# Kernel optimization log

Measured on AMD Instinct MI355X. Metric: run time of the kernel, lower is better.

## Reference

```python
import jax, jax.numpy as jnp
import numpy as np

NEG_SLOPE = 0.2  # PyG GATConv default negative_slope


def _gat_layer(x, src, dst, W_src, W_dst, att_src, att_dst, bias, num_nodes):
    """Single-head GATConv (concat=True, heads=1, add_self_loops=False)."""
    h_src = x @ W_src                      # [N, C]
    h_dst = x @ W_dst                      # [N, C]
    a_src = h_src @ att_src                # [N]
    a_dst = h_dst @ att_dst                # [N]
    # per-edge attention logits: message j -> i uses a_src[j] + a_dst[i]
    e = jax.nn.leaky_relu(a_src[src] + a_dst[dst], NEG_SLOPE)  # [E]
    # numerically stable softmax over incoming edges of each destination
    m = jax.ops.segment_max(e, dst, num_segments=num_nodes)    # [N]
    ee = jnp.exp(e - m[dst])                                   # [E]
    denom = jax.ops.segment_sum(ee, dst, num_segments=num_nodes)  # [N]
    alpha = ee / denom[dst]                                    # [E]
    # attention-weighted scatter-add of source messages
    out = jax.ops.segment_sum(h_src[src] * alpha[:, None], dst,
                              num_segments=num_nodes)          # [N, C]
    return out + bias


def setup_inputs() -> dict:
    key = jax.random.key(0)
    ks = jax.random.split(key, 12)
    N, E, F_IN, HID, OUT = 100000, 1600000, 128, 128, 64
    inp = {
        "x": jax.random.normal(ks[0], (N, F_IN), dtype=jnp.float32),
        "edge_index": jax.random.randint(ks[1], (2, E), 0, N, dtype=jnp.int64
                                         if jax.config.jax_enable_x64 else jnp.int32),
        "W_src1": jax.random.normal(ks[2], (F_IN, HID), dtype=jnp.float32) / np.sqrt(F_IN),
        "W_dst1": jax.random.normal(ks[3], (F_IN, HID), dtype=jnp.float32) / np.sqrt(F_IN),
        "att_src1": jax.random.normal(ks[4], (HID,), dtype=jnp.float32) / np.sqrt(HID),
        "att_dst1": jax.random.normal(ks[5], (HID,), dtype=jnp.float32) / np.sqrt(HID),
        "b1": jnp.zeros((HID,), dtype=jnp.float32),
        "W_src2": jax.random.normal(ks[6], (HID, OUT), dtype=jnp.float32) / np.sqrt(HID),
        "W_dst2": jax.random.normal(ks[7], (HID, OUT), dtype=jnp.float32) / np.sqrt(HID),
        "att_src2": jax.random.normal(ks[8], (OUT,), dtype=jnp.float32) / np.sqrt(OUT),
        "att_dst2": jax.random.normal(ks[9], (OUT,), dtype=jnp.float32) / np.sqrt(OUT),
        "b2": jnp.zeros((OUT,), dtype=jnp.float32),
    }
    return inp


def reference(x, edge_index, W_src1, W_dst1, att_src1, att_dst1, b1,
              W_src2, W_dst2, att_src2, att_dst2, b2):
    N = x.shape[0]
    src, dst = edge_index[0], edge_index[1]
    h = _gat_layer(x, src, dst, W_src1, W_dst1, att_src1, att_dst1, b1, N)
    h = jax.nn.relu(h)
    out = _gat_layer(h, src, dst, W_src2, W_dst2, att_src2, att_dst2, b2, N)
    return out
```

## Files before the change

kernel.cpp:

```cpp
#include <hip/hip_runtime.h>

#define F_IN 128
#define NEG_SLOPE 0.2f
#define SCAN_CHUNK 2048
#define CH 4096

typedef __attribute__((ext_vector_type(8))) short bf16x8;
typedef __attribute__((ext_vector_type(4))) float f32x4;

__device__ inline unsigned short f2bf(float f) {
    unsigned int u = __float_as_uint(f);
    unsigned int r = (u + 0x7fffu + ((u >> 16) & 1u)) >> 16;
    return (unsigned short)r;
}
__device__ inline float bf2f(unsigned short h) { return __uint_as_float((unsigned int)h << 16); }
__device__ inline float bflo(unsigned int u) { return __uint_as_float(u << 16); }
__device__ inline float bfhi(unsigned int u) { return __uint_as_float(u & 0xffff0000u); }

__device__ inline int bswiz(int n, int k) {
    int ct = n >> 4, rlo = n & 15, kk = k >> 5, q = (k >> 3) & 3, j = k & 7;
    return (((ct * 4 + kk) * 64 + q * 16 + rlo) << 3) + j;
}

__global__ void k_prep(const float* __restrict__ Ws1, const float* __restrict__ Wd1,
                       const float* __restrict__ as1, const float* __restrict__ ad1,
                       const float* __restrict__ Ws2, const float* __restrict__ Wd2,
                       const float* __restrict__ as2, const float* __restrict__ ad2,
                       float* __restrict__ vecs,
                       unsigned short* __restrict__ w1hi, unsigned short* __restrict__ w1lo,
                       unsigned short* __restrict__ w2hi, unsigned short* __restrict__ w2lo) {
    int bid = blockIdx.x, tid = threadIdx.x;
    if (bid == 0 && tid < 128) {
        int f = tid;
        float s1 = 0.f, d1 = 0.f, s2 = 0.f, d2 = 0.f;
        for (int c = 0; c < 128; ++c) {
            s1 += Ws1[f * 128 + c] * as1[c];
            d1 += Wd1[f * 128 + c] * ad1[c];
        }
        for (int c = 0; c < 64; ++c) {
            s2 += Ws2[f * 64 + c] * as2[c];
            d2 += Wd2[f * 64 + c] * ad2[c];
        }
        vecs[f] = s1; vecs[128 + f] = d1; vecs[256 + f] = s2; vecs[384 + f] = d2;
    } else if (bid >= 1 && bid < 65) {
        int idx = (bid - 1) * 256 + tid;
        int n = idx >> 7, k = idx & 127;
        float w = Ws1[k * 128 + n];
        unsigned short h = f2bf(w);
        int si = bswiz(n, k);
        w1hi[si] = h;
        w1lo[si] = f2bf(w - bf2f(h));
    } else if (bid >= 65 && bid < 97) {
        int idx = (bid - 65) * 256 + tid;
        int n = idx >> 7, k = idx & 127;
        float w = Ws2[k * 64 + n];
        unsigned short h = f2bf(w);
        int si = bswiz(n, k);
        w2hi[si] = h;
        w2lo[si] = f2bf(w - bf2f(h));
    }
}


__global__ void k_bhist(const int* __restrict__ dsts, int* __restrict__ table,
                        int E, int NB, int nblk) {
    __shared__ int bins[512];
    int t = threadIdx.x, blk = blockIdx.x;
    for (int j = t; j < NB; j += 256) bins[j] = 0;
    __syncthreads();
    int base = blk * CH;
    #pragma unroll
    for (int k = 0; k < CH / 256; ++k) {
        int idx = base + k * 256 + t;
        if (idx < E) atomicAdd(&bins[dsts[idx] >> 8], 1);
    }
    __syncthreads();
    for (int j = t; j < NB; j += 256) table[(long long)j * nblk + blk] = bins[j];
}

__global__ void k_blocksum2(const int* __restrict__ in, int* __restrict__ bsum, int M) {
    __shared__ int sh[256];
    int t = threadIdx.x;
    long long base = (long long)blockIdx.x * SCAN_CHUNK + (long long)t * 8;
    int s = 0;
    #pragma unroll
    for (int k = 0; k < 8; ++k) {
        long long i = base + k;
        if (i < M) s += in[i];
    }
    sh[t] = s;
    __syncthreads();
    for (int off = 128; off; off >>= 1) {
        if (t < off) sh[t] += sh[t + off];
        __syncthreads();
    }
    if (t == 0) bsum[blockIdx.x] = sh[0];
}

__global__ void k_scan2(const int* __restrict__ in, const int* __restrict__ bsum,
                        int* __restrict__ out, int M) {
    __shared__ int sh[256];
    int t = threadIdx.x, bid = blockIdx.x;
    int pre = 0;
    for (int b = 0; b < bid; ++b) pre += bsum[b];
    long long base = (long long)bid * SCAN_CHUNK + (long long)t * 8;
    int loc[8];
    int s = 0;
    #pragma unroll
    for (int k = 0; k < 8; ++k) {
        long long i = base + k;
        int v = (i < M) ? in[i] : 0;
        loc[k] = s;
        s += v;
    }
    sh[t] = s;
    __syncthreads();
    for (int off = 1; off < 256; off <<= 1) {
        int tmp = (t >= off) ? sh[t - off] : 0;
        __syncthreads();
        sh[t] += tmp;
        __syncthreads();
    }
    int toff = pre + sh[t] - s;
    #pragma unroll
    for (int k = 0; k < 8; ++k) {
        long long i = base + k;
        if (i < M) out[i] = toff + loc[k];
    }
}

__global__ void k_bscat(const int* __restrict__ srcs, const int* __restrict__ dsts,
                        const int* __restrict__ tscan, int2* __restrict__ pairA,
                        int E, int NB, int nblk) {
    __shared__ int offs[512];
    int t = threadIdx.x, blk = blockIdx.x;
    for (int j = t; j < NB; j += 256) offs[j] = tscan[(long long)j * nblk + blk];
    __syncthreads();
    int base = blk * CH;
    #pragma unroll
    for (int k = 0; k < CH / 256; ++k) {
        int idx = base + k * 256 + t;
        if (idx < E) {
            int d = dsts[idx], s = srcs[idx];
            int p = atomicAdd(&offs[d >> 8], 1);
            int2 pr; pr.x = d; pr.y = s;
            pairA[p] = pr;
        }
    }
}

__global__ void k_bfin(const int2* __restrict__ pairA, const int* __restrict__ tscan,
                       int* __restrict__ perm, int* __restrict__ rowptr,
                       int NB, int nblk, int N, int E) {
    __shared__ int scnt[256];
    __shared__ int sh[256];
    __shared__ int sptr[256];
    int t = threadIdx.x, b = blockIdx.x;
    int beg = tscan[(long long)b * nblk];
    int end = (b + 1 < NB) ? tscan[(long long)(b + 1) * nblk] : E;
    scnt[t] = 0;
    __syncthreads();
    for (int i = beg + t; i < end; i += 256) {
        int2 p = pairA[i];
        atomicAdd(&scnt[p.x & 255], 1);
    }
    __syncthreads();
    int c = scnt[t];
    sh[t] = c;
    __syncthreads();
    for (int off = 1; off < 256; off <<= 1) {
        int tmp = (t >= off) ? sh[t - off] : 0;
        __syncthreads();
        sh[t] += tmp;
        __syncthreads();
    }
    int excl = sh[t] - c;
    int node = (b << 8) + t;
    if (node < N) rowptr[node] = beg + excl;
    sptr[t] = beg + excl;
    __syncthreads();
    for (int i = beg + t; i < end; i += 256) {
        int2 p = pairA[i];
        int pos = atomicAdd(&sptr[p.x & 255], 1);
        perm[pos] = p.y;
    }
    if (b == NB - 1 && t == 0) rowptr[N] = E;
}

template <int COLS, bool ABF16>
__launch_bounds__(256)
__global__ void k_gemm_mfma(const void* __restrict__ Xv,
                            const unsigned short* __restrict__ Bh,
                            const unsigned short* __restrict__ Bl,
                            const float* __restrict__ vecs_s,
                            const float* __restrict__ vecs_d,
                            unsigned short* __restrict__ H,
                            float* __restrict__ a_s, float* __restrict__ a_d, int N) {
    int tid = threadIdx.x;
    int wave = tid >> 6, lane = tid & 63;
    int q = lane >> 4, rlo = lane & 15;
    long long wrow0 = (long long)blockIdx.x * 128 + wave * 32;

    bf16x8 Ahi[2][4], Alo[2][4];
    #pragma unroll
    for (int rt = 0; rt < 2; ++rt) {
        long long r = wrow0 + rt * 16 + rlo;
        long long rr = (r < N) ? r : (long long)(N - 1);
        float ps = 0.f, pd = 0.f;
        #pragma unroll
        for (int kk = 0; kk < 4; ++kk) {
            int k0 = kk * 32 + q * 8;
            float xv[8];
            if constexpr (ABF16) {
                const unsigned short* Xu = (const unsigned short*)Xv;
                bf16x8 av = *(const bf16x8*)(Xu + rr * 128 + k0);
                Ahi[rt][kk] = av;
                #pragma unroll
                for (int j = 0; j < 8; ++j) xv[j] = bf2f((unsigned short)av[j]);
            } else {
                const float* Xf = (const float*)Xv;
                float4 x0 = *(const float4*)(Xf + rr * 128 + k0);
                float4 x1 = *(const float4*)(Xf + rr * 128 + k0 + 4);
                xv[0] = x0.x; xv[1] = x0.y; xv[2] = x0.z; xv[3] = x0.w;
                xv[4] = x1.x; xv[5] = x1.y; xv[6] = x1.z; xv[7] = x1.w;
                bf16x8 ah, al;
                #pragma unroll
                for (int j = 0; j < 8; ++j) {
                    unsigned short h = f2bf(xv[j]);
                    ah[j] = (short)h;
                    al[j] = (short)f2bf(xv[j] - bf2f(h));
                }
                Ahi[rt][kk] = ah; Alo[rt][kk] = al;
            }
            float4 vs0 = *(const float4*)(vecs_s + k0);
            float4 vs1 = *(const float4*)(vecs_s + k0 + 4);
            float4 vd0 = *(const float4*)(vecs_d + k0);
            float4 vd1 = *(const float4*)(vecs_d + k0 + 4);
            ps += xv[0] * vs0.x + xv[1] * vs0.y + xv[2] * vs0.z + xv[3] * vs0.w
                + xv[4] * vs1.x + xv[5] * vs1.y + xv[6] * vs1.z + xv[7] * vs1.w;
            pd += xv[0] * vd0.x + xv[1] * vd0.y + xv[2] * vd0.z + xv[3] * vd0.w
                + xv[4] * vd1.x + xv[5] * vd1.y + xv[6] * vd1.z + xv[7] * vd1.w;
        }
        ps += __shfl_xor(ps, 16); ps += __shfl_xor(ps, 32);
        pd += __shfl_xor(pd, 16); pd += __shfl_xor(pd, 32);
        if (q == 0 && r < N) { a_s[r] = ps; a_d[r] = pd; }
    }

    const bf16x8* Bh8 = (const bf16x8*)Bh;
    const bf16x8* Bl8 = (const bf16x8*)Bl;
    #pragma unroll 1
    for (int ct = 0; ct < COLS / 16; ++ct) {
        bf16x8 bh[4], bl[4];
        #pragma unroll
        for (int kk = 0; kk < 4; ++kk) {
            bh[kk] = Bh8[(ct * 4 + kk) * 64 + lane];
            bl[kk] = Bl8[(ct * 4 + kk) * 64 + lane];
        }
        f32x4 acc0 = {0.f, 0.f, 0.f, 0.f};
        f32x4 acc1 = {0.f, 0.f, 0.f, 0.f};
        #pragma unroll
        for (int kk = 0; kk < 4; ++kk) {
            acc0 = __builtin_amdgcn_mfma_f32_16x16x32_bf16(Ahi[0][kk], bh[kk], acc0, 0, 0, 0);
            acc1 = __builtin_amdgcn_mfma_f32_16x16x32_bf16(Ahi[1][kk], bh[kk], acc1, 0, 0, 0);
            if constexpr (!ABF16) {
                acc0 = __builtin_amdgcn_mfma_f32_16x16x32_bf16(Alo[0][kk], bh[kk], acc0, 0, 0, 0);
                acc1 = __builtin_amdgcn_mfma_f32_16x16x32_bf16(Alo[1][kk], bh[kk], acc1, 0, 0, 0);
            }
            acc0 = __builtin_amdgcn_mfma_f32_16x16x32_bf16(Ahi[0][kk], bl[kk], acc0, 0, 0, 0);
            acc1 = __builtin_amdgcn_mfma_f32_16x16x32_bf16(Ahi[1][kk], bl[kk], acc1, 0, 0, 0);
        }
        #pragma unroll
        for (int i2 = 0; i2 < 4; ++i2) {
            long long o0 = wrow0 + q * 4 + i2;
            long long o1 = wrow0 + 16 + q * 4 + i2;
            if (o0 < N) H[o0 * COLS + ct * 16 + rlo] = f2bf(acc0[i2]);
            if (o1 < N) H[o1 * COLS + ct * 16 + rlo] = f2bf(acc1[i2]);
        }
    }
}

__launch_bounds__(256)
__global__ void k_agg128(const int* __restrict__ rowptr, const int* __restrict__ perm,
                         const float* __restrict__ a_s, const float* __restrict__ a_d,
                         const unsigned short* __restrict__ H, const float* __restrict__ bias,
                         unsigned short* __restrict__ out_bf, int N) {
    int wave = (int)(((long long)blockIdx.x * 256 + threadIdx.x) >> 6);
    int lane = threadIdx.x & 63;
    if (wave >= N) return;
    int beg = __builtin_amdgcn_readfirstlane(rowptr[wave]);
    int end = __builtin_amdgcn_readfirstlane(rowptr[wave + 1]);
    float ad = __uint_as_float(__builtin_amdgcn_readfirstlane(__float_as_uint(a_d[wave])));

    const unsigned int* H32 = (const unsigned int*)H;
    float acc0 = 0.f, acc1 = 0.f, wsum = 0.f;
    int i = beg;
    for (; i + 8 <= end; i += 8) {
        int s[8];
        unsigned int v[8];
        #pragma unroll
        for (int j = 0; j < 8; ++j)
            s[j] = __builtin_amdgcn_readfirstlane(perm[i + j]);
        #pragma unroll
        for (int j = 0; j < 8; ++j)
            v[j] = H32[(long long)s[j] * 64 + lane];
        #pragma unroll
        for (int j = 0; j < 8; ++j) {
            float t = a_s[s[j]] + ad;
            t = t > 0.f ? t : NEG_SLOPE * t;
            float w = __expf(t);
            acc0 += w * bflo(v[j]);
            acc1 += w * bfhi(v[j]);
            wsum += w;
        }
    }
    for (; i < end; ++i) {
        int s = __builtin_amdgcn_readfirstlane(perm[i]);
        unsigned int v = H32[(long long)s * 64 + lane];
        float t = a_s[s] + ad;
        t = t > 0.f ? t : NEG_SLOPE * t;
        float w = __expf(t);
        acc0 += w * bflo(v); acc1 += w * bfhi(v);
        wsum += w;
    }
    float inv = (wsum > 0.f) ? __fdividef(1.f, wsum) : 0.f;
    float o0 = fmaxf(acc0 * inv + bias[2 * lane], 0.f);
    float o1 = fmaxf(acc1 * inv + bias[2 * lane + 1], 0.f);
    unsigned int pk = (unsigned int)f2bf(o0) | ((unsigned int)f2bf(o1) << 16);
    ((unsigned int*)out_bf)[(long long)wave * 64 + lane] = pk;
}

__launch_bounds__(256)
__global__ void k_agg64(const int* __restrict__ rowptr, const int* __restrict__ perm,
                        const float* __restrict__ a_s, const float* __restrict__ a_d,
                        const unsigned short* __restrict__ H, const float* __restrict__ bias,
                        float* __restrict__ out, int N) {
    int wave = (int)(((long long)blockIdx.x * 256 + threadIdx.x) >> 6);
    int lane = threadIdx.x & 63;
    if (wave >= N) return;
    int c = lane & 31, h = lane >> 5;
    int beg = __builtin_amdgcn_readfirstlane(rowptr[wave]);
    int end = __builtin_amdgcn_readfirstlane(rowptr[wave + 1]);
    float ad = __uint_as_float(__builtin_amdgcn_readfirstlane(__float_as_uint(a_d[wave])));

    const unsigned int* H32 = (const unsigned int*)H;
    float acc0 = 0.f, acc1 = 0.f, wsum = 0.f;
    int base = beg;
    for (; base + 16 <= end; base += 16) {
        int s[8];
        unsigned int v[8];
        #pragma unroll
        for (int j = 0; j < 8; ++j)
            s[j] = perm[base + h + 2 * j];
        #pragma unroll
        for (int j = 0; j < 8; ++j)
            v[j] = H32[(long long)s[j] * 32 + c];
        #pragma unroll
        for (int j = 0; j < 8; ++j) {
            float t = a_s[s[j]] + ad;
            t = t > 0.f ? t : NEG_SLOPE * t;
            float w = __expf(t);
            acc0 += w * bflo(v[j]);
            acc1 += w * bfhi(v[j]);
            wsum += w;
        }
    }
    for (; base + 8 <= end; base += 8) {
        int s[4];
        unsigned int v[4];
        #pragma unroll
        for (int j = 0; j < 4; ++j)
            s[j] = perm[base + h + 2 * j];
        #pragma unroll
        for (int j = 0; j < 4; ++j)
            v[j] = H32[(long long)s[j] * 32 + c];
        #pragma unroll
        for (int j = 0; j < 4; ++j) {
            float t = a_s[s[j]] + ad;
            t = t > 0.f ? t : NEG_SLOPE * t;
            float w = __expf(t);
            acc0 += w * bflo(v[j]);
            acc1 += w * bfhi(v[j]);
            wsum += w;
        }
    }
    for (int i = base + h; i < end; i += 2) {
        int s = perm[i];
        unsigned int v = H32[(long long)s * 32 + c];
        float t = a_s[s] + ad;
        t = t > 0.f ? t : NEG_SLOPE * t;
        float w = __expf(t);
        acc0 += w * bflo(v); acc1 += w * bfhi(v);
        wsum += w;
    }
    acc0 += __shfl_xor(acc0, 32);
    acc1 += __shfl_xor(acc1, 32);
    wsum += __shfl_xor(wsum, 32);
    if (h == 0) {
        float inv = (wsum > 0.f) ? __fdividef(1.f, wsum) : 0.f;
        float2 o;
        o.x = acc0 * inv + bias[2 * c];
        o.y = acc1 * inv + bias[2 * c + 1];
        *(float2*)(out + (long long)wave * 64 + 2 * c) = o;
    }
}

extern "C" void kernel_launch(void* const* d_in, const int* in_sizes, int n_in,
                              void* d_out, int out_size, void* d_ws, size_t ws_size,
                              hipStream_t stream) {
    const float* x   = (const float*)d_in[0];
    const int*   ei  = (const int*)d_in[1];
    const float* Ws1 = (const float*)d_in[2];
    const float* Wd1 = (const float*)d_in[3];
    const float* as1 = (const float*)d_in[4];
    const float* ad1 = (const float*)d_in[5];
    const float* b1  = (const float*)d_in[6];
    const float* Ws2 = (const float*)d_in[7];
    const float* Wd2 = (const float*)d_in[8];
    const float* as2 = (const float*)d_in[9];
    const float* ad2 = (const float*)d_in[10];
    const float* b2  = (const float*)d_in[11];
    float* out = (float*)d_out;

    const int N = in_sizes[0] / F_IN;
    const int E = in_sizes[1] / 2;
    const int* srcs = ei;
    const int* dsts = ei + E;

    const int nblk = (E + CH - 1) / CH;
    const int NB   = (N + 255) >> 8;
    const int M    = NB * nblk;
    const int nb2  = (M + SCAN_CHUNK - 1) / SCAN_CHUNK;

    unsigned short* hbuf = (unsigned short*)d_ws;
    unsigned short* x2bf = hbuf + (size_t)N * 128;
    int*   perm   = (int*)(x2bf + (size_t)N * 128);
    float* a_s1   = (float*)(perm + E);
    float* a_d1   = a_s1 + N;
    float* a_s2   = a_d1 + N;
    float* a_d2   = a_s2 + N;
    int*   rowptr = (int*)(a_d2 + N);
    int*   table  = rowptr + N + 4;
    int*   tscan  = table + M + 4;
    int*   bsum   = tscan + M + 4;
    unsigned short* w1hi = (unsigned short*)(bsum + 128);
    unsigned short* w1lo = w1hi + 16384;
    unsigned short* w2hi = w1lo + 16384;
    unsigned short* w2lo = w2hi + 8192;
    float* vecs   = (float*)(w2lo + 8192);
    int2*  pairA  = (int2*)x2bf;

    k_prep<<<97, 256, 0, stream>>>(Ws1, Wd1, as1, ad1, Ws2, Wd2, as2, ad2,
                                   vecs, w1hi, w1lo, w2hi, w2lo);
    k_bhist<<<nblk, 256, 0, stream>>>(dsts, table, E, NB, nblk);
    k_blocksum2<<<nb2, 256, 0, stream>>>(table, bsum, M);
    k_scan2<<<nb2, 256, 0, stream>>>(table, bsum, tscan, M);
    k_bscat<<<nblk, 256, 0, stream>>>(srcs, dsts, tscan, pairA, E, NB, nblk);
    k_bfin<<<NB, 256, 0, stream>>>(pairA, tscan, perm, rowptr, NB, nblk, N, E);

    k_gemm_mfma<128, false><<<(N + 127) / 128, 256, 0, stream>>>(
        x, w1hi, w1lo, vecs, vecs + 128, hbuf, a_s1, a_d1, N);
    k_agg128<<<(N + 3) / 4, 256, 0, stream>>>(
        rowptr, perm, a_s1, a_d1, hbuf, b1, x2bf, N);

    k_gemm_mfma<64, true><<<(N + 127) / 128, 256, 0, stream>>>(
        x2bf, w2hi, w2lo, vecs + 256, vecs + 384, hbuf, a_s2, a_d2, N);
    k_agg64<<<(N + 3) / 4, 256, 0, stream>>>(
        rowptr, perm, a_s2, a_d2, hbuf, b2, out, N);
}
```

Measured before the change: 323.3 us.

## Precompute per-edge attention weights in separate kernel; pack CSR pairs into single ints

Adds a k_alpha kernel that computes the exp(leaky_relu(a_s+a_d)) weight for every edge into a buffer in CSR order. The aggregation kernels then stream these weights instead of gathering a_s and computing exp per edge. In the edge-sort path, k_bscat packs the (src, dst-low-byte) pair into one int instead of int2, and the prefix scan now runs in place on the table. k_agg128 also gains a 16-wide unrolled loop. The trade is an extra kernel launch per layer plus an extra E-sized write and read, against removing the random a_s gathers and the exp work from the gather-bound aggregation loops.

```diff
diff --git a/kernel.cpp b/kernel.cpp
--- a/kernel.cpp
+++ b/kernel.cpp
@@ -97,8 +97,7 @@
     if (t == 0) bsum[blockIdx.x] = sh[0];
 }
 
-__global__ void k_scan2(const int* __restrict__ in, const int* __restrict__ bsum,
-                        int* __restrict__ out, int M) {
+__global__ void k_scan2(int* __restrict__ io, const int* __restrict__ bsum, int M) {
     __shared__ int sh[256];
     int t = threadIdx.x, bid = blockIdx.x;
     int pre = 0;
@@ -109,7 +108,7 @@
     #pragma unroll
     for (int k = 0; k < 8; ++k) {
         long long i = base + k;
-        int v = (i < M) ? in[i] : 0;
+        int v = (i < M) ? io[i] : 0;
         loc[k] = s;
         s += v;
     }
@@ -125,16 +124,16 @@
     #pragma unroll
     for (int k = 0; k < 8; ++k) {
         long long i = base + k;
-        if (i < M) out[i] = toff + loc[k];
+        if (i < M) io[i] = toff + loc[k];
     }
 }
 
 __global__ void k_bscat(const int* __restrict__ srcs, const int* __restrict__ dsts,
-                        const int* __restrict__ tscan, int2* __restrict__ pairA,
+                        const int* __restrict__ table, int* __restrict__ pairA,
                         int E, int NB, int nblk) {
     __shared__ int offs[512];
     int t = threadIdx.x, blk = blockIdx.x;
-    for (int j = t; j < NB; j += 256) offs[j] = tscan[(long long)j * nblk + blk];
+    for (int j = t; j < NB; j += 256) offs[j] = table[(long long)j * nblk + blk];
     __syncthreads();
     int base = blk * CH;
     #pragma unroll
@@ -143,26 +142,24 @@
         if (idx < E) {
             int d = dsts[idx], s = srcs[idx];
             int p = atomicAdd(&offs[d >> 8], 1);
-            int2 pr; pr.x = d; pr.y = s;
-            pairA[p] = pr;
-        }
-    }
-}
-
-__global__ void k_bfin(const int2* __restrict__ pairA, const int* __restrict__ tscan,
+            pairA[p] = (s << 8) | (d & 255);
+        }
+    }
+}
+
+__global__ void k_bfin(const int* __restrict__ pairA, const int* __restrict__ table,
                        int* __restrict__ perm, int* __restrict__ rowptr,
                        int NB, int nblk, int N, int E) {
     __shared__ int scnt[256];
     __shared__ int sh[256];
     __shared__ int sptr[256];
     int t = threadIdx.x, b = blockIdx.x;
-    int beg = tscan[(long long)b * nblk];
-    int end = (b + 1 < NB) ? tscan[(long long)(b + 1) * nblk] : E;
+    int beg = table[(long long)b * nblk];
+    int end = (b + 1 < NB) ? table[(long long)(b + 1) * nblk] : E;
     scnt[t] = 0;
     __syncthreads();
     for (int i = beg + t; i < end; i += 256) {
-        int2 p = pairA[i];
-        atomicAdd(&scnt[p.x & 255], 1);
+        atomicAdd(&scnt[pairA[i] & 255], 1);
     }
     __syncthreads();
     int c = scnt[t];
@@ -180,11 +177,29 @@
     sptr[t] = beg + excl;
     __syncthreads();
     for (int i = beg + t; i < end; i += 256) {
-        int2 p = pairA[i];
-        int pos = atomicAdd(&sptr[p.x & 255], 1);
-        perm[pos] = p.y;
+        int u = pairA[i];
+        int pos = atomicAdd(&sptr[u & 255], 1);
+        perm[pos] = u >> 8;
     }
     if (b == NB - 1 && t == 0) rowptr[N] = E;
+}
+
+__launch_bounds__(256)
+__global__ void k_alpha(const int* __restrict__ rowptr, const int* __restrict__ perm,
+                        const float* __restrict__ a_s, const float* __restrict__ a_d,
+                        float* __restrict__ w, int N) {
+    long long wid = ((long long)blockIdx.x * 256 + threadIdx.x) >> 6;
+    int lane = threadIdx.x & 63;
+    int g = lane >> 4, l = lane & 15;
+    long long row = wid * 4 + g;
+    if (row >= N) return;
+    int beg = rowptr[row], end = rowptr[row + 1];
+    float ad = a_d[row];
+    for (int i = beg + l; i < end; i += 16) {
+        float t = a_s[perm[i]] + ad;
+        t = t > 0.f ? t : NEG_SLOPE * t;
+        w[i] = __expf(t);
+    }
 }
 
 template <int COLS, bool ABF16>
@@ -281,7 +296,7 @@
 
 __launch_bounds__(256)
 __global__ void k_agg128(const int* __restrict__ rowptr, const int* __restrict__ perm,
-                         const float* __restrict__ a_s, const float* __restrict__ a_d,
+                         const float* __restrict__ wbuf,
                          const unsigned short* __restrict__ H, const float* __restrict__ bias,
                          unsigned short* __restrict__ out_bf, int N) {
     int wave = (int)(((long long)blockIdx.x * 256 + threadIdx.x) >> 6);
@@ -289,36 +304,54 @@
     if (wave >= N) return;
     int beg = __builtin_amdgcn_readfirstlane(rowptr[wave]);
     int end = __builtin_amdgcn_readfirstlane(rowptr[wave + 1]);
-    float ad = __uint_as_float(__builtin_amdgcn_readfirstlane(__float_as_uint(a_d[wave])));
 
     const unsigned int* H32 = (const unsigned int*)H;
     float acc0 = 0.f, acc1 = 0.f, wsum = 0.f;
     int i = beg;
+    for (; i + 16 <= end; i += 16) {
+        int s[16];
+        float wv[16];
+        unsigned int v[16];
+        #pragma unroll
+        for (int j = 0; j < 16; ++j)
+            s[j] = __builtin_amdgcn_readfirstlane(perm[i + j]);
+        #pragma unroll
+        for (int j = 0; j < 16; ++j)
+            wv[j] = wbuf[i + j];
+        #pragma unroll
+        for (int j = 0; j < 16; ++j)
+            v[j] = H32[(long long)s[j] * 64 + lane];
+        #pragma unroll
+        for (int j = 0; j < 16; ++j) {
+            acc0 += wv[j] * bflo(v[j]);
+            acc1 += wv[j] * bfhi(v[j]);
+            wsum += wv[j];
+        }
+    }
     for (; i + 8 <= end; i += 8) {
         int s[8];
+        float wv[8];
         unsigned int v[8];
         #pragma unroll
         for (int j = 0; j < 8; ++j)
             s[j] = __builtin_amdgcn_readfirstlane(perm[i + j]);
         #pragma unroll
         for (int j = 0; j < 8; ++j)
+            wv[j] = wbuf[i + j];
+        #pragma unroll
+        for (int j = 0; j < 8; ++j)
             v[j] = H32[(long long)s[j] * 64 + lane];
         #pragma unroll
         for (int j = 0; j < 8; ++j) {
-            float t = a_s[s[j]] + ad;
-            t = t > 0.f ? t : NEG_SLOPE * t;
-            float w = __expf(t);
-            acc0 += w * bflo(v[j]);
-            acc1 += w * bfhi(v[j]);
-            wsum += w;
+            acc0 += wv[j] * bflo(v[j]);
+            acc1 += wv[j] * bfhi(v[j]);
+            wsum += wv[j];
         }
     }
     for (; i < end; ++i) {
         int s = __builtin_amdgcn_readfirstlane(perm[i]);
+        float w = wbuf[i];
         unsigned int v = H32[(long long)s * 64 + lane];
-        float t = a_s[s] + ad;
-        t = t > 0.f ? t : NEG_SLOPE * t;
-        float w = __expf(t);
         acc0 += w * bflo(v); acc1 += w * bfhi(v);
         wsum += w;
     }
@@ -331,7 +364,7 @@
 
 __launch_bounds__(256)
 __global__ void k_agg64(const int* __restrict__ rowptr, const int* __restrict__ perm,
-                        const float* __restrict__ a_s, const float* __restrict__ a_d,
+                        const float* __restrict__ wbuf,
                         const unsigned short* __restrict__ H, const float* __restrict__ bias,
                         float* __restrict__ out, int N) {
     int wave = (int)(((long long)blockIdx.x * 256 + threadIdx.x) >> 6);
@@ -340,55 +373,54 @@
     int c = lane & 31, h = lane >> 5;
     int beg = __builtin_amdgcn_readfirstlane(rowptr[wave]);
     int end = __builtin_amdgcn_readfirstlane(rowptr[wave + 1]);
-    float ad = __uint_as_float(__builtin_amdgcn_readfirstlane(__float_as_uint(a_d[wave])));
 
     const unsigned int* H32 = (const unsigned int*)H;
     float acc0 = 0.f, acc1 = 0.f, wsum = 0.f;
     int base = beg;
     for (; base + 16 <= end; base += 16) {
         int s[8];
+        float wv[8];
         unsigned int v[8];
         #pragma unroll
         for (int j = 0; j < 8; ++j)
             s[j] = perm[base + h + 2 * j];
         #pragma unroll
         for (int j = 0; j < 8; ++j)
+            wv[j] = wbuf[base + h + 2 * j];
+        #pragma unroll
+        for (int j = 0; j < 8; ++j)
             v[j] = H32[(long long)s[j] * 32 + c];
         #pragma unroll
         for (int j = 0; j < 8; ++j) {
-            float t = a_s[s[j]] + ad;
-            t = t > 0.f ? t : NEG_SLOPE * t;
-            float w = __expf(t);
-            acc0 += w * bflo(v[j]);
-            acc1 += w * bfhi(v[j]);
-            wsum += w;
+            acc0 += wv[j] * bflo(v[j]);
+            acc1 += wv[j] * bfhi(v[j]);
+            wsum += wv[j];
         }
     }
     for (; base + 8 <= end; base += 8) {
         int s[4];
+        float wv[4];
         unsigned int v[4];
         #pragma unroll
         for (int j = 0; j < 4; ++j)
             s[j] = perm[base + h + 2 * j];
         #pragma unroll
         for (int j = 0; j < 4; ++j)
+            wv[j] = wbuf[base + h + 2 * j];
+        #pragma unroll
+        for (int j = 0; j < 4; ++j)
             v[j] = H32[(long long)s[j] * 32 + c];
         #pragma unroll
         for (int j = 0; j < 4; ++j) {
-            float t = a_s[s[j]] + ad;
-            t = t > 0.f ? t : NEG_SLOPE * t;
-            float w = __expf(t);
-            acc0 += w * bflo(v[j]);
-            acc1 += w * bfhi(v[j]);
-            wsum += w;
+            acc0 += wv[j] * bflo(v[j]);
+            acc1 += wv[j] * bfhi(v[j]);
+            wsum += wv[j];
         }
     }
     for (int i = base + h; i < end; i += 2) {
         int s = perm[i];
+        float w = wbuf[i];
         unsigned int v = H32[(long long)s * 32 + c];
-        float t = a_s[s] + ad;
-        t = t > 0.f ? t : NEG_SLOPE * t;
-        float w = __expf(t);
         acc0 += w * bflo(v); acc1 += w * bfhi(v);
         wsum += w;
     }
@@ -438,32 +470,36 @@
     float* a_d1   = a_s1 + N;
     float* a_s2   = a_d1 + N;
     float* a_d2   = a_s2 + N;
-    int*   rowptr = (int*)(a_d2 + N);
-    int*   table  = rowptr + N + 4;
-    int*   tscan  = table + M + 4;
-    int*   bsum   = tscan + M + 4;
+    float* wbuf   = a_d2 + N;
+    int*   rowptr = (int*)(wbuf + E);
+    int*   bsum   = rowptr + N + 4;
     unsigned short* w1hi = (unsigned short*)(bsum + 128);
     unsigned short* w1lo = w1hi + 16384;
     unsigned short* w2hi = w1lo + 16384;
     unsigned short* w2lo = w2hi + 8192;
     float* vecs   = (float*)(w2lo + 8192);
-    int2*  pairA  = (int2*)x2bf;
+    int*   pairA  = (int*)x2bf;
+    int*   table  = pairA + E;
 
     k_prep<<<97, 256, 0, stream>>>(Ws1, Wd1, as1, ad1, Ws2, Wd2, as2, ad2,
                                    vecs, w1hi, w1lo, w2hi, w2lo);
     k_bhist<<<nblk, 256, 0, stream>>>(dsts, table, E, NB, nblk);
     k_blocksum2<<<nb2, 256, 0, stream>>>(table, bsum, M);
-    k_scan2<<<nb2, 256, 0, stream>>>(table, bsum, tscan, M);
-    k_bscat<<<nblk, 256, 0, stream>>>(srcs, dsts, tscan, pairA, E, NB, nblk);
-    k_bfin<<<NB, 256, 0, stream>>>(pairA, tscan, perm, rowptr, NB, nblk, N, E);
+    k_scan2<<<nb2, 256, 0, stream>>>(table, bsum, M);
+    k_bscat<<<nblk, 256, 0, stream>>>(srcs, dsts, table, pairA, E, NB, nblk);
+    k_bfin<<<NB, 256, 0, stream>>>(pairA, table, perm, rowptr, NB, nblk, N, E);
+
+    const int ablocks = (((N + 3) / 4) * 64 + 255) / 256;
 
     k_gemm_mfma<128, false><<<(N + 127) / 128, 256, 0, stream>>>(
         x, w1hi, w1lo, vecs, vecs + 128, hbuf, a_s1, a_d1, N);
+    k_alpha<<<ablocks, 256, 0, stream>>>(rowptr, perm, a_s1, a_d1, wbuf, N);
     k_agg128<<<(N + 3) / 4, 256, 0, stream>>>(
-        rowptr, perm, a_s1, a_d1, hbuf, b1, x2bf, N);
+        rowptr, perm, wbuf, hbuf, b1, x2bf, N);
 
     k_gemm_mfma<64, true><<<(N + 127) / 128, 256, 0, stream>>>(
         x2bf, w2hi, w2lo, vecs + 256, vecs + 384, hbuf, a_s2, a_d2, N);
+    k_alpha<<<ablocks, 256, 0, stream>>>(rowptr, perm, a_s2, a_d2, wbuf, N);
     k_agg64<<<(N + 3) / 4, 256, 0, stream>>>(
-        rowptr, perm, a_s2, a_d2, hbuf, b2, out, N);
-}
+        rowptr, perm, wbuf, hbuf, b2, out, N);
+}
```

Measured after the change: 345.5 us. +6.9%, slower.
